# Performance work log

Measured on AMD Instinct MI355X. Metric: run time of the kernel, lower is better.

Reference implementation:

```python
import math
import jax, jax.numpy as jnp
import numpy as np

N = 65536
S = 4            # n_scales
F = 64           # n_fourier
H = 256          # hidden
NB = 2           # res-blocks per branch (n_blocks=8 // n_scales=4)
IN_F = 2 + 8 * F # 514 fourier features per branch
OUT_DIM = 1
FREQ_MIN, FREQ_MAX = 1.0, 64.0


def setup_inputs() -> dict:
    key = jax.random.key(0)
    ks = jax.random.split(key, 10)
    xy = jax.random.uniform(ks[0], (N, 2), dtype=jnp.float32)
    # per-branch log-frequency init: linspace(log f_lo, log f_hi, F) within each scale band
    log_bounds = np.linspace(math.log(FREQ_MIN), math.log(FREQ_MAX), S + 1)
    w = np.stack([np.linspace(log_bounds[i], log_bounds[i + 1], F) for i in range(S)]).astype(np.float32)
    w_x = jnp.asarray(w)
    w_y = jnp.asarray(w)
    # NTK-parameterized linears: weight ~ N(0,1), bias = 0, scaled by 1/sqrt(fan_in) in forward
    proj_W = jax.random.normal(ks[1], (S, H, IN_F), dtype=jnp.float32)
    proj_b = jnp.zeros((S, H), dtype=jnp.float32)
    blk_W1 = jax.random.normal(ks[2], (S, NB, H, H), dtype=jnp.float32)
    blk_b1 = jnp.zeros((S, NB, H), dtype=jnp.float32)
    blk_W2 = jax.random.normal(ks[3], (S, NB, H, H), dtype=jnp.float32)
    blk_b2 = jnp.zeros((S, NB, H), dtype=jnp.float32)
    # head / shortcut are plain nn.Linear: use fan-in-scaled init baked into weights
    head_W = jax.random.normal(ks[4], (OUT_DIM, H), dtype=jnp.float32) / math.sqrt(H)
    head_b = jnp.zeros((OUT_DIM,), dtype=jnp.float32)
    sc_W = jax.random.normal(ks[5], (OUT_DIM, S * IN_F), dtype=jnp.float32) / math.sqrt(S * IN_F)
    return {"xy": xy, "w_x": w_x, "w_y": w_y, "proj_W": proj_W, "proj_b": proj_b,
            "blk_W1": blk_W1, "blk_b1": blk_b1, "blk_W2": blk_W2, "blk_b2": blk_b2,
            "head_W": head_W, "head_b": head_b, "sc_W": sc_W}


def _fourier(xy, w_x, w_y):
    # xy: [N,2]; w_x,w_y: [S,F] -> f: [S,N,2+8F]
    Bx = jnp.exp(w_x)[:, None, :]             # [S,1,F]
    By = jnp.exp(w_y)[:, None, :]
    px = jnp.pi * xy[None, :, 0:1] * Bx       # [S,N,F]
    py = jnp.pi * xy[None, :, 1:2] * By
    xy_b = jnp.broadcast_to(xy[None], (w_x.shape[0], xy.shape[0], 2))
    return jnp.concatenate([xy_b,
                            jnp.sin(px), jnp.cos(px),
                            jnp.sin(py), jnp.cos(py),
                            jnp.sin(px + py), jnp.cos(px + py),
                            jnp.sin(px - py), jnp.cos(px - py)], axis=-1)


def reference(xy, w_x, w_y, proj_W, proj_b, blk_W1, blk_b1, blk_W2, blk_b2, head_W, head_b, sc_W):
    gelu = lambda t: jax.nn.gelu(t, approximate=False)  # torch nn.GELU default = exact erf
    s_in = 1.0 / math.sqrt(IN_F)   # NTK scale for proj
    s_h = 1.0 / math.sqrt(H)       # NTK scale for block linears
    f = _fourier(xy, w_x, w_y)                                   # [S,N,IN_F]
    h = gelu(jnp.einsum('snf,shf->snh', f, proj_W) * s_in + proj_b[:, None, :])
    for b in range(NB):  # small fixed layer count
        t = gelu(jnp.einsum('snh,sgh->sng', h, blk_W1[:, b]) * s_h + blk_b1[:, b, None, :])
        h = h + jnp.einsum('sng,shg->snh', t, blk_W2[:, b]) * s_h + blk_b2[:, b, None, :]
    combined = jnp.sum(h, axis=0)                                # [N,H]
    out = combined @ head_W.T + head_b                           # [N,OUT_DIM]
    all_f = jnp.moveaxis(f, 0, 1).reshape(xy.shape[0], -1)       # [N, S*IN_F]
    return out + all_f @ sc_W.T
```

## Files before the change

kernel.cpp:

```cpp
#include <hip/hip_runtime.h>
#include <hip/hip_bf16.h>
#include <cmath>


#define NSC   4
#define NFREQ 64
#define HID   256
#define NBLK  2
#define INF   514
#define TM    64
#define NTHR  512

#define T_OFF    32768
#define SMEM_BYTES 65536

#define TILE_E   8192
#define PROJ_OFF(s)    ((s) * 131072)
#define W1_OFF   524288
#define W2_OFF   1048576
#define WSB_ELEMS 1572864

static constexpr float S_IN = 0.04411042041035620f;
static constexpr float S_H  = 0.0625f;
static constexpr float LOG2E = 1.4426950408889634f;

typedef __attribute__((ext_vector_type(8))) short bf16x8;
typedef __attribute__((ext_vector_type(4))) float f32x4;

__device__ __forceinline__ unsigned short f2bf(float v) {
  __hip_bfloat16 b = __float2bfloat16(v);
  unsigned short u;
  __builtin_memcpy(&u, &b, 2);
  return u;
}

__device__ __forceinline__ unsigned pack2(float a, float b) {
  return (unsigned)f2bf(a) | ((unsigned)f2bf(b) << 16);
}

__device__ __forceinline__ float geluf(float x) {
  const float z = fabsf(x) * 0.7071067811865476f;
  const float t = __builtin_amdgcn_rcpf(fmaf(0.3275911f, z, 1.0f));
  float p = 1.061405429f;
  p = fmaf(p, t, -1.453152027f);
  p = fmaf(p, t, 1.421413741f);
  p = fmaf(p, t, -0.284496736f);
  p = fmaf(p, t, 0.254829592f);
  const float e = __builtin_amdgcn_exp2f(-z * z * LOG2E);
  const float erf_ = 1.0f - p * t * e;
  return 0.5f * x * (1.0f + copysignf(erf_, x));
}

template<bool WS, bool PERM, int KSTEPS, int ROWB>
__device__ __forceinline__ void gemmK(const char* a_base,
                                      const unsigned short* __restrict__ wt,
                                      const float* __restrict__ wf,
                                      const int fp_rs, const int fp_co,
                                      const int lane, const int hq,
                                      f32x4 acc[2][4]) {
  const int ar = lane & 15;
  const int q  = lane >> 4;
  bf16x8 wb[3][2];

  auto loadw = [&](int ks, bf16x8 w[2]) {
#pragma unroll
    for (int hf = 0; hf < 2; ++hf) {
      const int row = hq * 32 + hf * 16 + ar;
      if constexpr (WS) {
        w[hf] = *(const bf16x8*)(wt + ks * TILE_E + row * 32 + q * 8);
      } else if constexpr (PERM) {
        const int j = ks * 4 + q;
        const float* p = wf + row * fp_rs + fp_co;
#pragma unroll
        for (int e = 0; e < 8; ++e) w[hf][e] = (short)f2bf(p[e * 64 + j]);
      } else {
        const float* p = wf + row * fp_rs + fp_co + ks * 32 + q * 8;
#pragma unroll
        for (int e = 0; e < 8; ++e) w[hf][e] = (short)f2bf(p[e]);
      }
    }
  };

  loadw(0, wb[0]);
  loadw(1, wb[1]);
#pragma unroll
  for (int ks = 0; ks < KSTEPS; ++ks) {
    if (ks + 2 < KSTEPS) loadw(ks + 2, wb[(ks + 2) % 3]);
    const bf16x8 w0 = wb[ks % 3][0];
    const bf16x8 w1 = wb[ks % 3][1];
    __builtin_amdgcn_s_setprio(1);
#pragma unroll
    for (int pr = 0; pr < 2; ++pr) {
      const int pt0 = (pr * 2) * 16 + ar;
      const int pt1 = (pr * 2 + 1) * 16 + ar;
      const int sl0 = (ks * 4 + q) ^ (pt0 & 7);
      const int sl1 = (ks * 4 + q) ^ (pt1 & 7);
      const bf16x8 a0 = *(const bf16x8*)(a_base + pt0 * ROWB + (sl0 << 4));
      const bf16x8 a1 = *(const bf16x8*)(a_base + pt1 * ROWB + (sl1 << 4));
      acc[0][pr * 2]     = __builtin_amdgcn_mfma_f32_16x16x32_bf16(w0, a0, acc[0][pr * 2], 0, 0, 0);
      acc[1][pr * 2]     = __builtin_amdgcn_mfma_f32_16x16x32_bf16(w1, a0, acc[1][pr * 2], 0, 0, 0);
      acc[0][pr * 2 + 1] = __builtin_amdgcn_mfma_f32_16x16x32_bf16(w0, a1, acc[0][pr * 2 + 1], 0, 0, 0);
      acc[1][pr * 2 + 1] = __builtin_amdgcn_mfma_f32_16x16x32_bf16(w1, a1, acc[1][pr * 2 + 1], 0, 0, 0);
    }
    __builtin_amdgcn_s_setprio(0);
  }
}

__global__ void cvt_weights(const float* __restrict__ projW,
                            const float* __restrict__ w1,
                            const float* __restrict__ w2,
                            unsigned short* __restrict__ o) {
  const int tot = WSB_ELEMS;
  for (int i = blockIdx.x * blockDim.x + threadIdx.x; i < tot;
       i += gridDim.x * blockDim.x) {
    float v;
    if (i < W1_OFF) {
      const int s = i >> 17, r = i & 131071;
      const int kst = r >> 13, rr = r & 8191;
      const int h = rr >> 5, kw = rr & 31;
      const int kp = kst * 32 + kw;
      const int j = kp >> 3, g = kp & 7;
      v = projW[(s * HID + h) * INF + 2 + g * 64 + j];
    } else if (i < W2_OFF) {
      const int i2 = i - W1_OFF;
      const int w = i2 >> 16, r = i2 & 65535;
      const int kst = r >> 13, h = (r >> 5) & 255, kw = r & 31;
      v = w1[w * 65536 + h * HID + kst * 32 + kw];
    } else {
      const int i2 = i - W2_OFF;
      const int w = i2 >> 16, r = i2 & 65535;
      const int kst = r >> 13, h = (r >> 5) & 255, kw = r & 31;
      v = w2[w * 65536 + h * HID + kst * 32 + kw];
    }
    o[i] = f2bf(v);
  }
}

template<bool WS>
__global__ __launch_bounds__(NTHR, 4)
void fnet_fused(const float* __restrict__ xy,
                const float* __restrict__ w_x,
                const float* __restrict__ w_y,
                const float* __restrict__ proj_W,
                const float* __restrict__ proj_b,
                const float* __restrict__ blk_W1,
                const float* __restrict__ blk_b1,
                const float* __restrict__ blk_W2,
                const float* __restrict__ blk_b2,
                const float* __restrict__ head_W,
                const float* __restrict__ head_b,
                const float* __restrict__ sc_W,
                const unsigned short* __restrict__ wsb,
                float* __restrict__ out) {
  extern __shared__ char smem[];
  char* f_arena = smem;
  char* h_base  = smem;
  char* t_base  = smem + T_OFF;

  const int tid  = threadIdx.x;
  const int lane = tid & 63;
  const int wave = tid >> 6;
  const int hq   = wave;
  const int m0   = blockIdx.x * TM;
  const int ar   = lane & 15;
  const int q    = lane >> 4;
  const float hb0 = head_b[0];

  auto tile_addr = [&](char* base, int hf, int pf) -> char* {
    const int pt = pf * 16 + ar;
    const int slot = (hq * 4 + hf * 2 + (q >> 1)) ^ (pt & 7);
    return base + pt * 512 + (slot << 4) + (q & 1) * 8;
  };

  f32x4 acc[2][4];
  auto zacc = [&]() {
#pragma unroll
    for (int a_ = 0; a_ < 2; ++a_)
#pragma unroll
      for (int b_ = 0; b_ < 4; ++b_) acc[a_][b_] = (f32x4)0.f;
  };

  for (int s = 0; s < NSC; ++s) {

    {
      const int fj = lane;
      const float bx = __builtin_amdgcn_exp2f(w_x[s * NFREQ + fj] * LOG2E);
      const float by = __builtin_amdgcn_exp2f(w_y[s * NFREQ + fj] * LOG2E);
      float sc8[8];
#pragma unroll
      for (int g2 = 0; g2 < 8; ++g2) sc8[g2] = sc_W[s * INF + 2 + g2 * NFREQ + fj];
      const float scW0 = sc_W[s * INF], scW1 = sc_W[s * INF + 1];
#pragma unroll 2
      for (int p = 0; p < 8; ++p) {
        const int pt = wave * 8 + p;
        const float x  = xy[(m0 + pt) * 2];
        const float yv = xy[(m0 + pt) * 2 + 1];
        float tx = 0.5f * x * bx;  tx -= floorf(tx);
        float ty = 0.5f * yv * by; ty -= floorf(ty);
        const float sx = __builtin_amdgcn_sinf(tx);
        const float cx = __builtin_amdgcn_cosf(tx);
        const float sy = __builtin_amdgcn_sinf(ty);
        const float cy = __builtin_amdgcn_cosf(ty);
        const float p1 = sx * cy, p2 = cx * sy, p3 = cx * cy, p4 = sx * sy;
        const float g0 = sx, g1 = cx, g2 = sy, g3 = cy;
        const float g4 = p1 + p2, g5 = p3 - p4, g6 = p1 - p2, g7 = p3 + p4;
        uint4 wv;
        wv.x = pack2(g0, g1); wv.y = pack2(g2, g3);
        wv.z = pack2(g4, g5); wv.w = pack2(g6, g7);
        *(uint4*)(f_arena + pt * 1024 + ((fj ^ (pt & 7)) << 4)) = wv;
        float psum = g0 * sc8[0] + g1 * sc8[1] + g2 * sc8[2] + g3 * sc8[3]
                   + g4 * sc8[4] + g5 * sc8[5] + g6 * sc8[6] + g7 * sc8[7];
        psum += __shfl_xor(psum, 1, 64);
        psum += __shfl_xor(psum, 2, 64);
        psum += __shfl_xor(psum, 4, 64);
        psum += __shfl_xor(psum, 8, 64);
        psum += __shfl_xor(psum, 16, 64);
        psum += __shfl_xor(psum, 32, 64);
        if (lane == 0)
          atomicAdd(&out[m0 + pt],
                    psum + x * scW0 + yv * scW1 + (s == 0 ? hb0 : 0.f));
      }
    }
    __syncthreads();

    zacc();
    gemmK<WS, true, 16, 1024>(f_arena, wsb + PROJ_OFF(s),
                              proj_W + s * HID * INF, INF, 2,
                              lane, hq, acc);
    __syncthreads();

#pragma unroll
    for (int hf = 0; hf < 2; ++hf) {
      const int Hb = hq * 32 + hf * 16 + 4 * q;
      const float4 pb4 = *(const float4*)(proj_b + s * HID + Hb);
      const float pbv[4] = {pb4.x, pb4.y, pb4.z, pb4.w};
      float wx0[4], wy0[4];
#pragma unroll
      for (int r = 0; r < 4; ++r) {
        const float2 w01 = *(const float2*)(proj_W + (size_t)(s * HID + Hb + r) * INF);
        wx0[r] = w01.x; wy0[r] = w01.y;
      }
#pragma unroll
      for (int pf = 0; pf < 4; ++pf) {
        const int pt = pf * 16 + ar;
        const float2 xp2 = *(const float2*)(xy + (m0 + pt) * 2);
        float hv[4];
#pragma unroll
        for (int r = 0; r < 4; ++r)
          hv[r] = geluf((acc[hf][pf][r] + xp2.x * wx0[r] + xp2.y * wy0[r]) * S_IN + pbv[r]);
        *(uint2*)tile_addr(h_base, hf, pf) =
            make_uint2(pack2(hv[0], hv[1]), pack2(hv[2], hv[3]));
      }
    }
    __syncthreads();

    for (int b = 0; b < NBLK; ++b) {
      const int wb_ = s * NBLK + b;
      zacc();
      gemmK<WS, false, 8, 512>(h_base, wsb + W1_OFF + wb_ * 65536,
                               blk_W1 + wb_ * 65536, HID, 0,
                               lane, hq, acc);
#pragma unroll
      for (int hf = 0; hf < 2; ++hf) {
        const int Hb = hq * 32 + hf * 16 + 4 * q;
        const float4 b14 = *(const float4*)(blk_b1 + wb_ * HID + Hb);
        const float b1v[4] = {b14.x, b14.y, b14.z, b14.w};
#pragma unroll
        for (int pf = 0; pf < 4; ++pf)
          *(uint2*)tile_addr(t_base, hf, pf) =
              make_uint2(pack2(geluf(acc[hf][pf][0] * S_H + b1v[0]),
                               geluf(acc[hf][pf][1] * S_H + b1v[1])),
                         pack2(geluf(acc[hf][pf][2] * S_H + b1v[2]),
                               geluf(acc[hf][pf][3] * S_H + b1v[3])));
      }
      __syncthreads();

      zacc();
      gemmK<WS, false, 8, 512>(t_base, wsb + W2_OFF + wb_ * 65536,
                               blk_W2 + wb_ * 65536, HID, 0,
                               lane, hq, acc);

      if (b + 1 < NBLK) {
#pragma unroll
        for (int hf = 0; hf < 2; ++hf) {
          const int Hb = hq * 32 + hf * 16 + 4 * q;
          const float4 b24 = *(const float4*)(blk_b2 + wb_ * HID + Hb);
          const float b2v[4] = {b24.x, b24.y, b24.z, b24.w};
#pragma unroll
          for (int pf = 0; pf < 4; ++pf) {
            const uint2 u = *(const uint2*)tile_addr(h_base, hf, pf);
            float hv[4];
            hv[0] = __uint_as_float(u.x << 16)         + acc[hf][pf][0] * S_H + b2v[0];
            hv[1] = __uint_as_float(u.x & 0xffff0000u) + acc[hf][pf][1] * S_H + b2v[1];
            hv[2] = __uint_as_float(u.y << 16)         + acc[hf][pf][2] * S_H + b2v[2];
            hv[3] = __uint_as_float(u.y & 0xffff0000u) + acc[hf][pf][3] * S_H + b2v[3];
            *(uint2*)tile_addr(h_base, hf, pf) =
                make_uint2(pack2(hv[0], hv[1]), pack2(hv[2], hv[3]));
          }
        }
      } else {
        float v[4] = {0.f, 0.f, 0.f, 0.f};
#pragma unroll
        for (int hf = 0; hf < 2; ++hf) {
          const int Hb = hq * 32 + hf * 16 + 4 * q;
          const float4 b24 = *(const float4*)(blk_b2 + wb_ * HID + Hb);
          const float4 hw4 = *(const float4*)(head_W + Hb);
#pragma unroll
          for (int pf = 0; pf < 4; ++pf) {
            const uint2 u = *(const uint2*)tile_addr(h_base, hf, pf);
            v[pf] += (__uint_as_float(u.x << 16)         + acc[hf][pf][0] * S_H + b24.x) * hw4.x
                   + (__uint_as_float(u.x & 0xffff0000u) + acc[hf][pf][1] * S_H + b24.y) * hw4.y
                   + (__uint_as_float(u.y << 16)         + acc[hf][pf][2] * S_H + b24.z) * hw4.z
                   + (__uint_as_float(u.y & 0xffff0000u) + acc[hf][pf][3] * S_H + b24.w) * hw4.w;
          }
        }
#pragma unroll
        for (int pf = 0; pf < 4; ++pf) {
          float vv = v[pf];
          vv += __shfl_xor(vv, 16, 64);
          vv += __shfl_xor(vv, 32, 64);
          if (lane < 16) atomicAdd(&out[m0 + pf * 16 + ar], vv);
        }
      }
      __syncthreads();
    }
  }
}

extern "C" void kernel_launch(void* const* d_in, const int* in_sizes, int n_in,
                              void* d_out, int out_size, void* d_ws, size_t ws_size,
                              hipStream_t stream) {
  (void)in_sizes; (void)n_in;
  const float* xy     = (const float*)d_in[0];
  const float* w_x    = (const float*)d_in[1];
  const float* w_y    = (const float*)d_in[2];
  const float* proj_W = (const float*)d_in[3];
  const float* proj_b = (const float*)d_in[4];
  const float* blk_W1 = (const float*)d_in[5];
  const float* blk_b1 = (const float*)d_in[6];
  const float* blk_W2 = (const float*)d_in[7];
  const float* blk_b2 = (const float*)d_in[8];
  const float* head_W = (const float*)d_in[9];
  const float* head_b = (const float*)d_in[10];
  const float* sc_W   = (const float*)d_in[11];
  float* out = (float*)d_out;

  const bool use_ws = ws_size >= (size_t)WSB_ELEMS * 2;
  const int nblocks = out_size / TM;

  (void)hipMemsetAsync(d_out, 0, (size_t)out_size * sizeof(float), stream);

  if (use_ws) {
    cvt_weights<<<768, 256, 0, stream>>>(proj_W, blk_W1, blk_W2,
                                         (unsigned short*)d_ws);
    fnet_fused<true><<<nblocks, NTHR, SMEM_BYTES, stream>>>(
        xy, w_x, w_y, proj_W, proj_b, blk_W1, blk_b1, blk_W2, blk_b2,
        head_W, head_b, sc_W, (const unsigned short*)d_ws, out);
  } else {
    fnet_fused<false><<<nblocks, NTHR, SMEM_BYTES, stream>>>(
        xy, w_x, w_y, proj_W, proj_b, blk_W1, blk_b1, blk_W2, blk_b2,
        head_W, head_b, sc_W, (const unsigned short*)nullptr, out);
  }
}
```

Measured before the change: 332.9 us.

## Defer shortcut and head reductions to kernel end; shrink weight prefetch to double buffer

Per-scale shortcut partial sums and head outputs now accumulate in registers and are reduced with shuffles and atomics once at the end of the kernel. Previously this happened inside every scale and block iteration. This cuts shuffle chains and global atomics from 4x to 1x per point. Separately, the GEMM weight prefetch drops from three buffers to two. That frees registers but leaves less latency hiding for global weight loads, and the unrolled psc[8] and hsum[4] arrays add register pressure.

```diff
diff --git a/kernel.cpp b/kernel.cpp
--- a/kernel.cpp
+++ b/kernel.cpp
@@ -60,7 +60,7 @@
                                       f32x4 acc[2][4]) {
   const int ar = lane & 15;
   const int q  = lane >> 4;
-  bf16x8 wb[3][2];
+  bf16x8 wb[2][2];
 
   auto loadw = [&](int ks, bf16x8 w[2]) {
 #pragma unroll
@@ -82,12 +82,11 @@
   };
 
   loadw(0, wb[0]);
-  loadw(1, wb[1]);
 #pragma unroll
   for (int ks = 0; ks < KSTEPS; ++ks) {
-    if (ks + 2 < KSTEPS) loadw(ks + 2, wb[(ks + 2) % 3]);
-    const bf16x8 w0 = wb[ks % 3][0];
-    const bf16x8 w1 = wb[ks % 3][1];
+    if (ks + 1 < KSTEPS) loadw(ks + 1, wb[(ks + 1) & 1]);
+    const bf16x8 w0 = wb[ks & 1][0];
+    const bf16x8 w1 = wb[ks & 1][1];
     __builtin_amdgcn_s_setprio(1);
 #pragma unroll
     for (int pr = 0; pr < 2; ++pr) {
@@ -180,8 +179,12 @@
       for (int b_ = 0; b_ < 4; ++b_) acc[a_][b_] = (f32x4)0.f;
   };
 
+  float psc[8];
+  float hsum[4] = {0.f, 0.f, 0.f, 0.f};
+#pragma unroll
+  for (int p = 0; p < 8; ++p) psc[p] = 0.f;
+
   for (int s = 0; s < NSC; ++s) {
-
     {
       const int fj = lane;
       const float bx = __builtin_amdgcn_exp2f(w_x[s * NFREQ + fj] * LOG2E);
@@ -208,17 +211,9 @@
         wv.x = pack2(g0, g1); wv.y = pack2(g2, g3);
         wv.z = pack2(g4, g5); wv.w = pack2(g6, g7);
         *(uint4*)(f_arena + pt * 1024 + ((fj ^ (pt & 7)) << 4)) = wv;
-        float psum = g0 * sc8[0] + g1 * sc8[1] + g2 * sc8[2] + g3 * sc8[3]
-                   + g4 * sc8[4] + g5 * sc8[5] + g6 * sc8[6] + g7 * sc8[7];
-        psum += __shfl_xor(psum, 1, 64);
-        psum += __shfl_xor(psum, 2, 64);
-        psum += __shfl_xor(psum, 4, 64);
-        psum += __shfl_xor(psum, 8, 64);
-        psum += __shfl_xor(psum, 16, 64);
-        psum += __shfl_xor(psum, 32, 64);
-        if (lane == 0)
-          atomicAdd(&out[m0 + pt],
-                    psum + x * scW0 + yv * scW1 + (s == 0 ? hb0 : 0.f));
+        psc[p] += g0 * sc8[0] + g1 * sc8[1] + g2 * sc8[2] + g3 * sc8[3]
+                + g4 * sc8[4] + g5 * sc8[5] + g6 * sc8[6] + g7 * sc8[7];
+        if (fj == 0) psc[p] += x * scW0 + yv * scW1;
       }
     }
     __syncthreads();
@@ -299,7 +294,6 @@
           }
         }
       } else {
-        float v[4] = {0.f, 0.f, 0.f, 0.f};
 #pragma unroll
         for (int hf = 0; hf < 2; ++hf) {
           const int Hb = hq * 32 + hf * 16 + 4 * q;
@@ -308,22 +302,34 @@
 #pragma unroll
           for (int pf = 0; pf < 4; ++pf) {
             const uint2 u = *(const uint2*)tile_addr(h_base, hf, pf);
-            v[pf] += (__uint_as_float(u.x << 16)         + acc[hf][pf][0] * S_H + b24.x) * hw4.x
-                   + (__uint_as_float(u.x & 0xffff0000u) + acc[hf][pf][1] * S_H + b24.y) * hw4.y
-                   + (__uint_as_float(u.y << 16)         + acc[hf][pf][2] * S_H + b24.z) * hw4.z
-                   + (__uint_as_float(u.y & 0xffff0000u) + acc[hf][pf][3] * S_H + b24.w) * hw4.w;
+            hsum[pf] += (__uint_as_float(u.x << 16)         + acc[hf][pf][0] * S_H + b24.x) * hw4.x
+                      + (__uint_as_float(u.x & 0xffff0000u) + acc[hf][pf][1] * S_H + b24.y) * hw4.y
+                      + (__uint_as_float(u.y << 16)         + acc[hf][pf][2] * S_H + b24.z) * hw4.z
+                      + (__uint_as_float(u.y & 0xffff0000u) + acc[hf][pf][3] * S_H + b24.w) * hw4.w;
           }
         }
-#pragma unroll
-        for (int pf = 0; pf < 4; ++pf) {
-          float vv = v[pf];
-          vv += __shfl_xor(vv, 16, 64);
-          vv += __shfl_xor(vv, 32, 64);
-          if (lane < 16) atomicAdd(&out[m0 + pf * 16 + ar], vv);
-        }
       }
       __syncthreads();
     }
+  }
+
+#pragma unroll
+  for (int pf = 0; pf < 4; ++pf) {
+    float vv = hsum[pf];
+    vv += __shfl_xor(vv, 16, 64);
+    vv += __shfl_xor(vv, 32, 64);
+    if (lane < 16) atomicAdd(&out[m0 + pf * 16 + ar], vv);
+  }
+#pragma unroll
+  for (int p = 0; p < 8; ++p) {
+    float v = psc[p];
+    v += __shfl_xor(v, 1, 64);
+    v += __shfl_xor(v, 2, 64);
+    v += __shfl_xor(v, 4, 64);
+    v += __shfl_xor(v, 8, 64);
+    v += __shfl_xor(v, 16, 64);
+    v += __shfl_xor(v, 32, 64);
+    if (lane == 0) atomicAdd(&out[m0 + wave * 8 + p], v + hb0);
   }
 }
 
```

Measured after the change: 344.0 us. 3.3% more time.
